# Kernel optimization log

Measured on AMD Instinct MI355X. Metric: run time of the kernel, lower is better.

The kernel has to match this reference:

```python
import jax, jax.numpy as jnp
import numpy as np

N_NODES = 100000


def _gcn_conv(h, src, dst, W, b, n_nodes):
    """PyG GCNConv with add_self_loops=True, symmetric normalization.
    out = D^-1/2 (A + I) D^-1/2 (h W) + b, aggregating src->dst."""
    h = h @ W  # transform first (out_dim <= in_dim), as PyG does
    ones = jnp.ones(src.shape[0], dtype=h.dtype)
    deg = jax.ops.segment_sum(ones, dst, num_segments=n_nodes) + 1.0  # +1 self loop
    dinv = jax.lax.rsqrt(deg)
    coef = dinv[src] * dinv[dst]  # per-edge norm
    agg = jax.ops.segment_sum(h[src] * coef[:, None], dst, num_segments=n_nodes)
    agg = agg + h * (dinv * dinv)[:, None]  # self-loop term: dinv_i^2 * h_i
    return agg + b


def setup_inputs() -> dict:
    key = jax.random.key(0)
    k1, k2, k3, k4 = jax.random.split(key, 4)
    x = jax.random.normal(k1, (N_NODES, 256), dtype=jnp.float32)
    edge_index = jax.random.randint(k2, (2, 1600000), 0, N_NODES, dtype=jnp.int64)
    W1 = jax.random.normal(k3, (256, 128), dtype=jnp.float32) * (1.0 / np.sqrt(256))
    b1 = jnp.zeros((128,), dtype=jnp.float32)
    W2 = jax.random.normal(k4, (128, 64), dtype=jnp.float32) * (1.0 / np.sqrt(128))
    b2 = jnp.zeros((64,), dtype=jnp.float32)
    return {"x": x, "edge_index": edge_index, "W1": W1, "b1": b1, "W2": W2, "b2": b2}


def reference(x, edge_index, W1, b1, W2, b2):
    src, dst = edge_index[0], edge_index[1]
    h = jax.nn.relu(_gcn_conv(x, src, dst, W1, b1, N_NODES))
    # dropout is identity in eval mode
    h = _gcn_conv(h, src, dst, W2, b2, N_NODES)
    return jax.nn.log_softmax(h, axis=1)
```

## Files before the change

kernel.cpp:

```cpp
#include <hip/hip_runtime.h>
#include <hip/hip_bf16.h>


#define N_NODES 100000
#define F_IN 256
#define F_MID 128
#define F_OUT 64

#define BSHIFT 8
#define BNODES 256
#define NBUCKETS ((N_NODES + BNODES - 1) / BNODES)
#define BCAP 6144
#define EPB 4096

typedef __attribute__((ext_vector_type(8))) short short8;
typedef __attribute__((ext_vector_type(4))) float f32x4;

__device__ inline ushort bf16_rne(float f) {
    uint u = __float_as_uint(f);
    u += 0x7FFF + ((u >> 16) & 1);
    return (ushort)(u >> 16);
}
__device__ inline float lo16(uint r) { return __uint_as_float(r << 16); }
__device__ inline float hi16(uint r) { return __uint_as_float(r & 0xffff0000u); }
__device__ inline uint pack_bf2(float a, float b) {
    return (uint)bf16_rne(a) | ((uint)bf16_rne(b) << 16);
}


__global__ __launch_bounds__(256)
void bucket_scatter_kernel(const int* __restrict__ src, const int* __restrict__ dst,
                           int* __restrict__ bcur, uint* __restrict__ ebuf, int E) {
    __shared__ int curL[NBUCKETS];
    int t = threadIdx.x;
    int e0 = blockIdx.x * EPB;
    int e1 = e0 + EPB; if (e1 > E) e1 = E;

    for (int i = t; i < NBUCKETS; i += 256) curL[i] = 0;
    __syncthreads();
    for (int i = e0 + t; i < e1; i += 256) atomicAdd(&curL[dst[i] >> BSHIFT], 1);
    __syncthreads();
    for (int i = t; i < NBUCKETS; i += 256) {
        int h = curL[i];
        curL[i] = h ? atomicAdd(&bcur[i], h) : 0;
    }
    __syncthreads();
    for (int i = e0 + t; i < e1; i += 256) {
        int d = dst[i], s = src[i];
        int b = d >> BSHIFT;
        int pos = atomicAdd(&curL[b], 1);
        if (pos < BCAP) ebuf[(size_t)b * BCAP + pos] = ((uint)(d & (BNODES - 1)) << 17) | (uint)s;
    }
}

__global__ __launch_bounds__(256)
void bucket_sort_kernel(const uint* __restrict__ ebuf, const int* __restrict__ bcur,
                        int* __restrict__ ssrc, int* __restrict__ rs, int* __restrict__ cnt,
                        float* __restrict__ dinv, int n) {
    __shared__ uint eL[BCAP];
    __shared__ int hist[BNODES], ps[BNODES];
    int b = blockIdx.x, t = threadIdx.x;
    int nb = bcur[b];
    if (nb > BCAP) nb = BCAP;
    for (int i = t; i < nb; i += 256) eL[i] = ebuf[(size_t)b * BCAP + i];
    hist[t] = 0;
    __syncthreads();
    for (int i = t; i < nb; i += 256) atomicAdd(&hist[eL[i] >> 17], 1);
    __syncthreads();
    ps[t] = hist[t];
    __syncthreads();
#pragma unroll
    for (int off = 1; off < BNODES; off <<= 1) {
        int v = (t >= off) ? ps[t - off] : 0;
        __syncthreads();
        ps[t] += v;
        __syncthreads();
    }
    int excl = ps[t] - hist[t];
    int node = b * BNODES + t;
    if (node < n) {
        rs[node] = b * BCAP + excl;
        cnt[node] = hist[t];
        dinv[node] = 1.0f / sqrtf((float)hist[t] + 1.0f);
    }
    __syncthreads();
    ps[t] = excl;
    __syncthreads();
    for (int i = t; i < nb; i += 256) {
        uint e = eL[i];
        int d = e >> 17;
        int p = atomicAdd(&ps[d], 1);
        ssrc[(size_t)b * BCAP + p] = (int)(e & 0x1FFFF);
    }
}

__global__ __launch_bounds__(256)
void wprep_kernel(const float* __restrict__ W1, const float* __restrict__ W2,
                  short8* __restrict__ W1f, short8* __restrict__ W2f) {
    int b = blockIdx.x;
    if (b < 16) {
        int f = b * 256 + threadIdx.x;
        int k0 = f >> 9, nt = (f >> 6) & 7, ln = f & 63;
        int kbase = k0 * 32 + (ln >> 4) * 8;
        int n = nt * 16 + (ln & 15);
        short8 fr;
#pragma unroll
        for (int j = 0; j < 8; ++j) fr[j] = (short)bf16_rne(W1[(kbase + j) * F_MID + n]);
        W1f[f] = fr;
    } else {
        int f = (b - 16) * 256 + threadIdx.x;
        int k0 = f >> 8, nt = (f >> 6) & 3, ln = f & 63;
        int kbase = k0 * 32 + (ln >> 4) * 8;
        int n = nt * 16 + (ln & 15);
        short8 fr;
#pragma unroll
        for (int j = 0; j < 8; ++j) fr[j] = (short)bf16_rne(W2[(kbase + j) * F_OUT + n]);
        W2f[f] = fr;
    }
}


__global__ __launch_bounds__(256)
void gemm1_kernel(const float* __restrict__ A, const short8* __restrict__ Wf,
                  const float* __restrict__ dinv, ushort* __restrict__ C,
                  int M, int nTiles) {
    __shared__ short8 BsF[4096];
    int tid = threadIdx.x;
    int lane = tid & 63, w = tid >> 6;
    for (int f = tid; f < 4096; f += 256) BsF[f] = Wf[f];
    __syncthreads();

    for (int t = blockIdx.x; t < nTiles; t += gridDim.x) {
        int m0 = t * 128 + w * 32;
        f32x4 acc[2][8];
#pragma unroll
        for (int mt = 0; mt < 2; ++mt)
#pragma unroll
            for (int nt = 0; nt < 8; ++nt) acc[mt][nt] = (f32x4){0.f, 0.f, 0.f, 0.f};

        for (int k0 = 0; k0 < 8; ++k0) {
            short8 afr[2];
#pragma unroll
            for (int mt = 0; mt < 2; ++mt) {
                int m = m0 + mt * 16 + (lane & 15);
                int k = k0 * 32 + (lane >> 4) * 8;
                short8 af = (short8){0, 0, 0, 0, 0, 0, 0, 0};
                if (m < M) {
                    const float4* ap = (const float4*)&A[(size_t)m * F_IN + k];
                    float4 v0 = ap[0], v1 = ap[1];
                    af[0] = (short)bf16_rne(v0.x); af[1] = (short)bf16_rne(v0.y);
                    af[2] = (short)bf16_rne(v0.z); af[3] = (short)bf16_rne(v0.w);
                    af[4] = (short)bf16_rne(v1.x); af[5] = (short)bf16_rne(v1.y);
                    af[6] = (short)bf16_rne(v1.z); af[7] = (short)bf16_rne(v1.w);
                }
                afr[mt] = af;
            }
#pragma unroll
            for (int nt = 0; nt < 8; ++nt) {
                short8 bfr = BsF[(k0 * 8 + nt) * 64 + lane];
                acc[0][nt] = __builtin_amdgcn_mfma_f32_16x16x32_bf16(afr[0], bfr, acc[0][nt], 0, 0, 0);
                acc[1][nt] = __builtin_amdgcn_mfma_f32_16x16x32_bf16(afr[1], bfr, acc[1][nt], 0, 0, 0);
            }
        }
#pragma unroll
        for (int mt = 0; mt < 2; ++mt)
#pragma unroll
            for (int i = 0; i < 4; ++i) {
                int r = m0 + mt * 16 + (lane >> 4) * 4 + i;
                if (r < M) {
                    float dv = dinv[r];
#pragma unroll
                    for (int nt = 0; nt < 8; ++nt)
                        C[(size_t)r * F_MID + nt * 16 + (lane & 15)] = bf16_rne(dv * acc[mt][nt][i]);
                }
            }
    }
}

__global__ __launch_bounds__(256)
void gemm2_kernel(const ushort* __restrict__ A, const short8* __restrict__ Wf,
                  const float* __restrict__ dinv, ushort* __restrict__ C,
                  int M, int nTiles) {
    __shared__ short8 BsF[1024];
    int tid = threadIdx.x;
    int lane = tid & 63, w = tid >> 6;
    for (int f = tid; f < 1024; f += 256) BsF[f] = Wf[f];
    __syncthreads();

    for (int t = blockIdx.x; t < nTiles; t += gridDim.x) {
        int m0 = t * 128 + w * 32;
        f32x4 acc[2][4];
#pragma unroll
        for (int mt = 0; mt < 2; ++mt)
#pragma unroll
            for (int nt = 0; nt < 4; ++nt) acc[mt][nt] = (f32x4){0.f, 0.f, 0.f, 0.f};

        for (int k0 = 0; k0 < 4; ++k0) {
            short8 afr[2];
#pragma unroll
            for (int mt = 0; mt < 2; ++mt) {
                int m = m0 + mt * 16 + (lane & 15);
                int k = k0 * 32 + (lane >> 4) * 8;
                short8 af = (short8){0, 0, 0, 0, 0, 0, 0, 0};
                if (m < M) af = *(const short8*)&A[(size_t)m * F_MID + k];
                afr[mt] = af;
            }
#pragma unroll
            for (int nt = 0; nt < 4; ++nt) {
                short8 bfr = BsF[(k0 * 4 + nt) * 64 + lane];
                acc[0][nt] = __builtin_amdgcn_mfma_f32_16x16x32_bf16(afr[0], bfr, acc[0][nt], 0, 0, 0);
                acc[1][nt] = __builtin_amdgcn_mfma_f32_16x16x32_bf16(afr[1], bfr, acc[1][nt], 0, 0, 0);
            }
        }
#pragma unroll
        for (int mt = 0; mt < 2; ++mt)
#pragma unroll
            for (int i = 0; i < 4; ++i) {
                int r = m0 + mt * 16 + (lane >> 4) * 4 + i;
                if (r < M) {
                    float dv = dinv[r];
#pragma unroll
                    for (int nt = 0; nt < 4; ++nt)
                        C[(size_t)r * F_OUT + nt * 16 + (lane & 15)] = bf16_rne(dv * acc[mt][nt][i]);
                }
            }
    }
}

__global__ __launch_bounds__(256)
void agg1_kernel(const uint4* __restrict__ h, const int* __restrict__ rs,
                 const int* __restrict__ cnt, const int* __restrict__ ssrc,
                 const float* __restrict__ dinv, const float* __restrict__ bias,
                 uint4* __restrict__ outp, int n) {
    int w = threadIdx.x >> 6, lane = threadIdx.x & 63;
    int node = blockIdx.x * 4 + w;
    if (node >= n) return;
    int q = lane >> 4, c16 = lane & 15;
    int start = rs[node], c = cnt[node];
    float dn = dinv[node];
    float a[8];
#pragma unroll
    for (int i = 0; i < 8; ++i) a[i] = 0.f;

    for (int base = 0; base < c; base += 4) {
        int eidx = base + q;
        if (eidx < c) {
            int s = ssrc[start + eidx];
            uint4 r = h[(size_t)s * 16 + c16];
            a[0] += lo16(r.x); a[1] += hi16(r.x);
            a[2] += lo16(r.y); a[3] += hi16(r.y);
            a[4] += lo16(r.z); a[5] += hi16(r.z);
            a[6] += lo16(r.w); a[7] += hi16(r.w);
        }
    }
#pragma unroll
    for (int i = 0; i < 8; ++i) {
        a[i] += __shfl_xor(a[i], 16);
        a[i] += __shfl_xor(a[i], 32);
    }
    uint4 sr = h[(size_t)node * 16 + c16];
    const float4* b4 = (const float4*)bias;
    float4 b0 = b4[c16 * 2], b1 = b4[c16 * 2 + 1];
    float o0 = fmaxf(fmaf(dn, a[0] + lo16(sr.x), b0.x), 0.f);
    float o1 = fmaxf(fmaf(dn, a[1] + hi16(sr.x), b0.y), 0.f);
    float o2 = fmaxf(fmaf(dn, a[2] + lo16(sr.y), b0.z), 0.f);
    float o3 = fmaxf(fmaf(dn, a[3] + hi16(sr.y), b0.w), 0.f);
    float o4 = fmaxf(fmaf(dn, a[4] + lo16(sr.z), b1.x), 0.f);
    float o5 = fmaxf(fmaf(dn, a[5] + hi16(sr.z), b1.y), 0.f);
    float o6 = fmaxf(fmaf(dn, a[6] + lo16(sr.w), b1.z), 0.f);
    float o7 = fmaxf(fmaf(dn, a[7] + hi16(sr.w), b1.w), 0.f);
    if (q == 0) {
        uint4 ov;
        ov.x = pack_bf2(o0, o1);
        ov.y = pack_bf2(o2, o3);
        ov.z = pack_bf2(o4, o5);
        ov.w = pack_bf2(o6, o7);
        outp[(size_t)node * 16 + c16] = ov;
    }
}

__global__ __launch_bounds__(256)
void agg2_kernel(const uint2* __restrict__ h, const int* __restrict__ rs,
                 const int* __restrict__ cnt, const int* __restrict__ ssrc,
                 const float* __restrict__ dinv, const float* __restrict__ bias,
                 float4* __restrict__ out4, int n) {
    int w = threadIdx.x >> 6, lane = threadIdx.x & 63;
    int node = blockIdx.x * 4 + w;
    if (node >= n) return;
    int q = lane >> 4, c16 = lane & 15;
    int start = rs[node], c = cnt[node];
    float dn = dinv[node];
    float a[4];
#pragma unroll
    for (int i = 0; i < 4; ++i) a[i] = 0.f;

    for (int base = 0; base < c; base += 4) {
        int eidx = base + q;
        if (eidx < c) {
            int s = ssrc[start + eidx];
            uint2 r = h[(size_t)s * 16 + c16];
            a[0] += lo16(r.x); a[1] += hi16(r.x);
            a[2] += lo16(r.y); a[3] += hi16(r.y);
        }
    }
#pragma unroll
    for (int i = 0; i < 4; ++i) {
        a[i] += __shfl_xor(a[i], 16);
        a[i] += __shfl_xor(a[i], 32);
    }
    uint2 sr = h[(size_t)node * 16 + c16];
    float4 bv = ((const float4*)bias)[c16];
    float v0 = fmaf(dn, a[0] + lo16(sr.x), bv.x);
    float v1 = fmaf(dn, a[1] + hi16(sr.x), bv.y);
    float v2 = fmaf(dn, a[2] + lo16(sr.y), bv.z);
    float v3 = fmaf(dn, a[3] + hi16(sr.y), bv.w);
    float m = fmaxf(fmaxf(v0, v1), fmaxf(v2, v3));
#pragma unroll
    for (int off = 1; off < 16; off <<= 1) m = fmaxf(m, __shfl_xor(m, off));
    float ssum = expf(v0 - m) + expf(v1 - m) + expf(v2 - m) + expf(v3 - m);
#pragma unroll
    for (int off = 1; off < 16; off <<= 1) ssum += __shfl_xor(ssum, off);
    float lg = m + logf(ssum);
    if (q == 0) out4[(size_t)node * 16 + c16] = make_float4(v0 - lg, v1 - lg, v2 - lg, v3 - lg);
}


extern "C" void kernel_launch(void* const* d_in, const int* in_sizes, int n_in,
                              void* d_out, int out_size, void* d_ws, size_t ws_size,
                              hipStream_t stream) {
    const float* x  = (const float*)d_in[0];
    const int*   ei = (const int*)d_in[1];
    const float* W1 = (const float*)d_in[2];
    const float* b1 = (const float*)d_in[3];
    const float* W2 = (const float*)d_in[4];
    const float* b2 = (const float*)d_in[5];
    float* out = (float*)d_out;

    const int N = N_NODES;
    const int E = in_sizes[1] / 2;
    const int* src = ei;
    const int* dst = ei + E;

    char* ws = (char*)d_ws;
    size_t off = 0;
    auto alloc = [&](size_t bytes) {
        char* p = ws + off;
        off = (off + bytes + 255) & ~(size_t)255;
        return p;
    };
    int*    bcur   = (int*)alloc(NBUCKETS * 4);
    int*    rs     = (int*)alloc(N * 4);
    int*    cnt    = (int*)alloc(N * 4);
    float*  dinv   = (float*)alloc(N * 4);
    short8* W1f    = (short8*)alloc(4096 * 16);
    short8* W2f    = (short8*)alloc(1024 * 16);
    uint*   ebuf   = (uint*)alloc((size_t)NBUCKETS * BCAP * 4);
    int*    ssrc   = (int*)alloc((size_t)NBUCKETS * BCAP * 4);
    uint*   h1     = (uint*)alloc((size_t)N * 64 * 4);
    uint*   h1a    = (uint*)alloc((size_t)N * 64 * 4);
    ushort* h2     = (ushort*)h1;

    const int nScatBlocks = (E + EPB - 1) / EPB;
    const int nAggBlocks  = (N + 3) / 4;
    const int nTiles      = (N + 127) / 128;
    const int nGemmGrid   = 512;

    hipMemsetAsync(bcur, 0, NBUCKETS * 4, stream);
    wprep_kernel<<<20, 256, 0, stream>>>(W1, W2, W1f, W2f);

    bucket_scatter_kernel<<<nScatBlocks, 256, 0, stream>>>(src, dst, bcur, ebuf, E);
    bucket_sort_kernel<<<NBUCKETS, 256, 0, stream>>>(ebuf, bcur, ssrc, rs, cnt, dinv, N);

    gemm1_kernel<<<nGemmGrid, 256, 0, stream>>>(x, W1f, dinv, (ushort*)h1, N, nTiles);
    agg1_kernel<<<nAggBlocks, 256, 0, stream>>>((const uint4*)h1, rs, cnt, ssrc, dinv, b1,
                                                (uint4*)h1a, N);
    gemm2_kernel<<<nGemmGrid, 256, 0, stream>>>((const ushort*)h1a, W2f, dinv, h2, N, nTiles);
    agg2_kernel<<<nAggBlocks, 256, 0, stream>>>((const uint2*)h2, rs, cnt, ssrc, dinv, b2,
                                                (float4*)out, N);
}
```

Baseline: 417.8 us.

## Restructure GEMM kernels: one tile per block, 512 threads, prefetched A loads

Both dense transform kernels drop the persistent grid-stride loop and launch one 128-row tile per block with 512 threads, each wave handling 16 rows instead of 32. This halves per-wave accumulator registers to raise occupancy and latency hiding. gemm1 software-prefetches the next K-slice of A while converting and issuing MFMAs for the current one, and gemm2 hoists all A loads ahead of the MFMA loop. The cost is that every block reloads the weight fragments into LDS, about 782 blocks instead of 512.

New measurement: 412.0 us. Within noise of the previous version (-1.4%).

```diff
diff --git a/kernel.cpp b/kernel.cpp
--- a/kernel.cpp
+++ b/kernel.cpp
@@ -120,110 +120,99 @@
 }
 
 
-__global__ __launch_bounds__(256)
+__global__ __launch_bounds__(512, 4)
 void gemm1_kernel(const float* __restrict__ A, const short8* __restrict__ Wf,
                   const float* __restrict__ dinv, ushort* __restrict__ C,
-                  int M, int nTiles) {
+                  int M) {
     __shared__ short8 BsF[4096];
     int tid = threadIdx.x;
     int lane = tid & 63, w = tid >> 6;
-    for (int f = tid; f < 4096; f += 256) BsF[f] = Wf[f];
-    __syncthreads();
-
-    for (int t = blockIdx.x; t < nTiles; t += gridDim.x) {
-        int m0 = t * 128 + w * 32;
-        f32x4 acc[2][8];
-#pragma unroll
-        for (int mt = 0; mt < 2; ++mt)
-#pragma unroll
-            for (int nt = 0; nt < 8; ++nt) acc[mt][nt] = (f32x4){0.f, 0.f, 0.f, 0.f};
-
-        for (int k0 = 0; k0 < 8; ++k0) {
-            short8 afr[2];
-#pragma unroll
-            for (int mt = 0; mt < 2; ++mt) {
-                int m = m0 + mt * 16 + (lane & 15);
-                int k = k0 * 32 + (lane >> 4) * 8;
-                short8 af = (short8){0, 0, 0, 0, 0, 0, 0, 0};
-                if (m < M) {
-                    const float4* ap = (const float4*)&A[(size_t)m * F_IN + k];
-                    float4 v0 = ap[0], v1 = ap[1];
-                    af[0] = (short)bf16_rne(v0.x); af[1] = (short)bf16_rne(v0.y);
-                    af[2] = (short)bf16_rne(v0.z); af[3] = (short)bf16_rne(v0.w);
-                    af[4] = (short)bf16_rne(v1.x); af[5] = (short)bf16_rne(v1.y);
-                    af[6] = (short)bf16_rne(v1.z); af[7] = (short)bf16_rne(v1.w);
-                }
-                afr[mt] = af;
-            }
-#pragma unroll
-            for (int nt = 0; nt < 8; ++nt) {
-                short8 bfr = BsF[(k0 * 8 + nt) * 64 + lane];
-                acc[0][nt] = __builtin_amdgcn_mfma_f32_16x16x32_bf16(afr[0], bfr, acc[0][nt], 0, 0, 0);
-                acc[1][nt] = __builtin_amdgcn_mfma_f32_16x16x32_bf16(afr[1], bfr, acc[1][nt], 0, 0, 0);
-            }
-        }
-#pragma unroll
-        for (int mt = 0; mt < 2; ++mt)
-#pragma unroll
-            for (int i = 0; i < 4; ++i) {
-                int r = m0 + mt * 16 + (lane >> 4) * 4 + i;
-                if (r < M) {
-                    float dv = dinv[r];
-#pragma unroll
-                    for (int nt = 0; nt < 8; ++nt)
-                        C[(size_t)r * F_MID + nt * 16 + (lane & 15)] = bf16_rne(dv * acc[mt][nt][i]);
-                }
-            }
-    }
-}
-
-__global__ __launch_bounds__(256)
+    for (int f = tid; f < 4096; f += 512) BsF[f] = Wf[f];
+    __syncthreads();
+
+    const float4 z4 = make_float4(0.f, 0.f, 0.f, 0.f);
+    int m0 = blockIdx.x * 128 + w * 16;
+    int m = m0 + (lane & 15);
+    bool mOk = (m < M);
+    const float4* aptr = (const float4*)&A[(size_t)(mOk ? m : 0) * F_IN + (lane >> 4) * 8];
+
+    f32x4 acc[8];
+#pragma unroll
+    for (int nt = 0; nt < 8; ++nt) acc[nt] = (f32x4){0.f, 0.f, 0.f, 0.f};
+
+    float4 v0 = mOk ? aptr[0] : z4;
+    float4 v1 = mOk ? aptr[1] : z4;
+
+#pragma unroll
+    for (int k0 = 0; k0 < 8; ++k0) {
+        short8 af;
+        af[0] = (short)bf16_rne(v0.x); af[1] = (short)bf16_rne(v0.y);
+        af[2] = (short)bf16_rne(v0.z); af[3] = (short)bf16_rne(v0.w);
+        af[4] = (short)bf16_rne(v1.x); af[5] = (short)bf16_rne(v1.y);
+        af[6] = (short)bf16_rne(v1.z); af[7] = (short)bf16_rne(v1.w);
+        if (k0 < 7) {
+            v0 = mOk ? aptr[(k0 + 1) * 8 + 0] : z4;
+            v1 = mOk ? aptr[(k0 + 1) * 8 + 1] : z4;
+        }
+#pragma unroll
+        for (int nt = 0; nt < 8; ++nt) {
+            short8 bfr = BsF[(k0 * 8 + nt) * 64 + lane];
+            acc[nt] = __builtin_amdgcn_mfma_f32_16x16x32_bf16(af, bfr, acc[nt], 0, 0, 0);
+        }
+    }
+#pragma unroll
+    for (int i = 0; i < 4; ++i) {
+        int r = m0 + (lane >> 4) * 4 + i;
+        if (r < M) {
+            float dv = dinv[r];
+#pragma unroll
+            for (int nt = 0; nt < 8; ++nt)
+                C[(size_t)r * F_MID + nt * 16 + (lane & 15)] = bf16_rne(dv * acc[nt][i]);
+        }
+    }
+}
+
+__global__ __launch_bounds__(512, 4)
 void gemm2_kernel(const ushort* __restrict__ A, const short8* __restrict__ Wf,
                   const float* __restrict__ dinv, ushort* __restrict__ C,
-                  int M, int nTiles) {
+                  int M) {
     __shared__ short8 BsF[1024];
     int tid = threadIdx.x;
     int lane = tid & 63, w = tid >> 6;
-    for (int f = tid; f < 1024; f += 256) BsF[f] = Wf[f];
-    __syncthreads();
-
-    for (int t = blockIdx.x; t < nTiles; t += gridDim.x) {
-        int m0 = t * 128 + w * 32;
-        f32x4 acc[2][4];
-#pragma unroll
-        for (int mt = 0; mt < 2; ++mt)
-#pragma unroll
-            for (int nt = 0; nt < 4; ++nt) acc[mt][nt] = (f32x4){0.f, 0.f, 0.f, 0.f};
-
-        for (int k0 = 0; k0 < 4; ++k0) {
-            short8 afr[2];
-#pragma unroll
-            for (int mt = 0; mt < 2; ++mt) {
-                int m = m0 + mt * 16 + (lane & 15);
-                int k = k0 * 32 + (lane >> 4) * 8;
-                short8 af = (short8){0, 0, 0, 0, 0, 0, 0, 0};
-                if (m < M) af = *(const short8*)&A[(size_t)m * F_MID + k];
-                afr[mt] = af;
-            }
-#pragma unroll
-            for (int nt = 0; nt < 4; ++nt) {
-                short8 bfr = BsF[(k0 * 4 + nt) * 64 + lane];
-                acc[0][nt] = __builtin_amdgcn_mfma_f32_16x16x32_bf16(afr[0], bfr, acc[0][nt], 0, 0, 0);
-                acc[1][nt] = __builtin_amdgcn_mfma_f32_16x16x32_bf16(afr[1], bfr, acc[1][nt], 0, 0, 0);
-            }
-        }
-#pragma unroll
-        for (int mt = 0; mt < 2; ++mt)
-#pragma unroll
-            for (int i = 0; i < 4; ++i) {
-                int r = m0 + mt * 16 + (lane >> 4) * 4 + i;
-                if (r < M) {
-                    float dv = dinv[r];
-#pragma unroll
-                    for (int nt = 0; nt < 4; ++nt)
-                        C[(size_t)r * F_OUT + nt * 16 + (lane & 15)] = bf16_rne(dv * acc[mt][nt][i]);
-                }
-            }
+    for (int f = tid; f < 1024; f += 512) BsF[f] = Wf[f];
+    __syncthreads();
+
+    int m0 = blockIdx.x * 128 + w * 16;
+    int m = m0 + (lane & 15);
+    bool mOk = (m < M);
+
+    f32x4 acc[4];
+#pragma unroll
+    for (int nt = 0; nt < 4; ++nt) acc[nt] = (f32x4){0.f, 0.f, 0.f, 0.f};
+
+    short8 afr[4];
+#pragma unroll
+    for (int k0 = 0; k0 < 4; ++k0) {
+        short8 af = (short8){0, 0, 0, 0, 0, 0, 0, 0};
+        if (mOk) af = *(const short8*)&A[(size_t)m * F_MID + k0 * 32 + (lane >> 4) * 8];
+        afr[k0] = af;
+    }
+#pragma unroll
+    for (int k0 = 0; k0 < 4; ++k0)
+#pragma unroll
+        for (int nt = 0; nt < 4; ++nt) {
+            short8 bfr = BsF[(k0 * 4 + nt) * 64 + lane];
+            acc[nt] = __builtin_amdgcn_mfma_f32_16x16x32_bf16(afr[k0], bfr, acc[nt], 0, 0, 0);
+        }
+#pragma unroll
+    for (int i = 0; i < 4; ++i) {
+        int r = m0 + (lane >> 4) * 4 + i;
+        if (r < M) {
+            float dv = dinv[r];
+#pragma unroll
+            for (int nt = 0; nt < 4; ++nt)
+                C[(size_t)r * F_OUT + nt * 16 + (lane & 15)] = bf16_rne(dv * acc[nt][i]);
+        }
     }
 }
 
@@ -363,7 +352,6 @@
     const int nScatBlocks = (E + EPB - 1) / EPB;
     const int nAggBlocks  = (N + 3) / 4;
     const int nTiles      = (N + 127) / 128;
-    const int nGemmGrid   = 512;
 
     hipMemsetAsync(bcur, 0, NBUCKETS * 4, stream);
     wprep_kernel<<<20, 256, 0, stream>>>(W1, W2, W1f, W2f);
@@ -371,10 +359,10 @@
     bucket_scatter_kernel<<<nScatBlocks, 256, 0, stream>>>(src, dst, bcur, ebuf, E);
     bucket_sort_kernel<<<NBUCKETS, 256, 0, stream>>>(ebuf, bcur, ssrc, rs, cnt, dinv, N);
 
-    gemm1_kernel<<<nGemmGrid, 256, 0, stream>>>(x, W1f, dinv, (ushort*)h1, N, nTiles);
+    gemm1_kernel<<<nTiles, 512, 0, stream>>>(x, W1f, dinv, (ushort*)h1, N);
     agg1_kernel<<<nAggBlocks, 256, 0, stream>>>((const uint4*)h1, rs, cnt, ssrc, dinv, b1,
                                                 (uint4*)h1a, N);
-    gemm2_kernel<<<nGemmGrid, 256, 0, stream>>>((const ushort*)h1a, W2f, dinv, h2, N, nTiles);
+    gemm2_kernel<<<nTiles, 512, 0, stream>>>((const ushort*)h1a, W2f, dinv, h2, N);
     agg2_kernel<<<nAggBlocks, 256, 0, stream>>>((const uint2*)h2, rs, cnt, ssrc, dinv, b2,
                                                 (float4*)out, N);
 }
```
